# Kernel optimization log

Measured on AMD Instinct MI355X. Metric: run time of the kernel, lower is better.

Reference implementation:

```python
import jax, jax.numpy as jnp
import numpy as np

N, E, IN, H, C, ED = 100000, 1600000, 128, 4, 32, 16
HC = H * C
NEG_SLOPE = 0.2
EPS = 1e-5


def setup_inputs() -> dict:
    key = jax.random.key(0)
    ks = jax.random.split(key, 12)
    x = jax.random.normal(ks[0], (N, IN), jnp.float32)
    edge_index = jax.random.randint(ks[1], (2, E), 0, N, dtype=jnp.int32)
    edge_attr = jax.random.normal(ks[2], (E, ED), jnp.float32)
    s_in = 1.0 / np.sqrt(IN)
    s_ed = 1.0 / np.sqrt(ED)
    s_c = 1.0 / np.sqrt(C)
    Wl = jax.random.normal(ks[3], (IN, HC), jnp.float32) * s_in
    bl = jnp.zeros((HC,), jnp.float32)
    Wr = jax.random.normal(ks[4], (IN, HC), jnp.float32) * s_in
    br = jnp.zeros((HC,), jnp.float32)
    We = jax.random.normal(ks[5], (ED, HC), jnp.float32) * s_ed
    att = jax.random.normal(ks[6], (H, C), jnp.float32) * s_c
    bias = jnp.zeros((HC,), jnp.float32)
    ln_weight = jnp.ones((HC,), jnp.float32)
    ln_bias = jnp.zeros((HC,), jnp.float32)
    return {"x": x, "edge_index": edge_index, "edge_attr": edge_attr,
            "Wl": Wl, "bl": bl, "Wr": Wr, "br": br, "We": We,
            "att": att, "bias": bias, "ln_weight": ln_weight, "ln_bias": ln_bias}


def gatv2_block(x, src, dst, edge_attr, Wl, bl, Wr, br, We, att, bias, ln_weight, ln_bias):
    n = x.shape[0]
    xl = (x @ Wl + bl).reshape(n, H, C)  # source-side transform
    xr = (x @ Wr + br).reshape(n, H, C)  # target-side transform
    # add_self_loops with fill_value='mean': self-loop edge_attr = mean of
    # incoming edge_attr per node (0 for isolated nodes)
    ea_sum = jax.ops.segment_sum(edge_attr, dst, num_segments=n)
    cnt = jax.ops.segment_sum(jnp.ones((edge_attr.shape[0],), edge_attr.dtype), dst, num_segments=n)
    self_attr = ea_sum / jnp.maximum(cnt, 1.0)[:, None]
    loop = jnp.arange(n, dtype=src.dtype)
    src_a = jnp.concatenate([src, loop])
    dst_a = jnp.concatenate([dst, loop])
    ea_a = jnp.concatenate([edge_attr, self_attr], axis=0)
    e_emb = (ea_a @ We).reshape(-1, H, C)
    # GATv2 attention: a^T LeakyReLU(xl_j + xr_i + e)
    m = xl[src_a] + xr[dst_a] + e_emb            # [Etot, H, C]
    m = jax.nn.leaky_relu(m, NEG_SLOPE)
    alpha = jnp.einsum('ehc,hc->eh', m, att)     # [Etot, H]
    amax = jax.ops.segment_max(alpha, dst_a, num_segments=n)
    alpha = jnp.exp(alpha - amax[dst_a])
    denom = jax.ops.segment_sum(alpha, dst_a, num_segments=n)
    alpha = alpha / denom[dst_a]
    out = jax.ops.segment_sum(xl[src_a] * alpha[:, :, None], dst_a, num_segments=n)
    h = out.reshape(n, HC) + bias
    # residual (in_dim == H*C so no projection), PyG graph-mode LayerNorm
    z = x + h
    mu = jnp.mean(z)
    var = jnp.mean((z - mu) ** 2)
    z = (z - mu) / jnp.sqrt(var + EPS)
    z = z * ln_weight + ln_bias
    return jax.nn.relu(z)  # dropout = identity in eval


def reference(x, edge_index, edge_attr, Wl, bl, Wr, br, We, att, bias, ln_weight, ln_bias):
    src, dst = edge_index[0], edge_index[1]
    return gatv2_block(x, src, dst, edge_attr, Wl, bl, Wr, br, We, att, bias, ln_weight, ln_bias)
```

## Files before the change

kernel.cpp:

```cpp
#include <hip/hip_runtime.h>
#include <hip/hip_bf16.h>

static constexpr float NEG_SLOPE = 0.2f;
static constexpr float LN_EPS = 1e-5f;

typedef float v2f __attribute__((ext_vector_type(2)));
typedef __attribute__((ext_vector_type(8))) short bf16x8;
typedef __attribute__((ext_vector_type(4))) float f32x4;

__device__ __forceinline__ unsigned f2b(float f) {
  unsigned u = __float_as_uint(f);
  return (u + 0x7fffu + ((u >> 16) & 1u)) >> 16;
}
__device__ __forceinline__ v2f b2f2(ushort2 u) {
  v2f r;
  r.x = __uint_as_float((unsigned)u.x << 16);
  r.y = __uint_as_float((unsigned)u.y << 16);
  return r;
}
__device__ __forceinline__ float sbl(unsigned w) {
  return __uint_as_float(w << 16);
}
__device__ __forceinline__ float sbh(unsigned w) {
  return __uint_as_float(w & 0xFFFF0000u);
}

__device__ __forceinline__ float head_sum16(float x) {
  float t;
  t = __int_as_float(__builtin_amdgcn_update_dpp(
      0, __float_as_int(x), 0xB1, 0xF, 0xF, true));
  x += t;
  t = __int_as_float(__builtin_amdgcn_update_dpp(
      0, __float_as_int(x), 0x4E, 0xF, 0xF, true));
  x += t;
  t = __int_as_float(__builtin_amdgcn_update_dpp(
      0, __float_as_int(x), 0x124, 0xF, 0xF, true));
  x += t;
  t = __int_as_float(__builtin_amdgcn_update_dpp(
      0, __float_as_int(x), 0x128, 0xF, 0xF, true));
  x += t;
  return x;
}

__global__ __launch_bounds__(256) void k_packB(
    const float* __restrict__ Wl, const float* __restrict__ Wr,
    const float* __restrict__ bl, const float* __restrict__ br,
    ushort* __restrict__ Bpack, float* __restrict__ bcat)
{
  int tid = blockIdx.x * 256 + threadIdx.x;
  int l = tid & 63, s = (tid >> 6) & 3, t = tid >> 8;
  int col = t * 16 + (l & 15);
  int kb = s * 32 + (l >> 4) * 8;
  const float* __restrict__ W = (col < 128) ? Wl : Wr;
  int c = col & 127;
  unsigned p[4];
#pragma unroll
  for (int i = 0; i < 4; ++i) {
    unsigned lo = f2b(W[(size_t)(kb + 2 * i) * 128 + c]);
    unsigned hi = f2b(W[(size_t)(kb + 2 * i + 1) * 128 + c]);
    p[i] = lo | (hi << 16);
  }
  *(uint4*)(Bpack + (size_t)tid * 8) = make_uint4(p[0], p[1], p[2], p[3]);
  if (tid < 256) bcat[tid] = (tid < 128) ? bl[tid] : br[tid - 128];
}

__global__ __launch_bounds__(256) void k_gemm_mfma(
    const float* __restrict__ x, const ushort* __restrict__ Bpack,
    const float* __restrict__ bcat, ushort* __restrict__ xl,
    float* __restrict__ outz, int n)
{
  const int lane = threadIdx.x & 63;
  const int w = threadIdx.x >> 6;
  const int row0 = blockIdx.x * 64 + w * 16;
  const int rowA = min(row0 + (lane & 15), n - 1);
  const int kgrp = lane >> 4;

  f32x4 acc[16];
#pragma unroll
  for (int t = 0; t < 16; ++t) acc[t] = (f32x4){0.f, 0.f, 0.f, 0.f};

#pragma unroll
  for (int s = 0; s < 4; ++s) {
    const float4* ap =
        (const float4*)(x + (size_t)rowA * 128 + s * 32 + kgrp * 8);
    float4 a0 = ap[0], a1 = ap[1];
    bf16x8 a;
    a[0] = (short)f2b(a0.x); a[1] = (short)f2b(a0.y);
    a[2] = (short)f2b(a0.z); a[3] = (short)f2b(a0.w);
    a[4] = (short)f2b(a1.x); a[5] = (short)f2b(a1.y);
    a[6] = (short)f2b(a1.z); a[7] = (short)f2b(a1.w);
#pragma unroll
    for (int t = 0; t < 16; ++t) {
      bf16x8 b =
          *(const bf16x8*)(Bpack + (((size_t)t * 4 + s) * 64 + lane) * 8);
      acc[t] = __builtin_amdgcn_mfma_f32_16x16x32_bf16(a, b, acc[t], 0, 0, 0);
    }
  }

  const int colg = lane & 15;
  const int rbase = row0 + (lane >> 4) * 4;
#pragma unroll
  for (int t = 0; t < 16; ++t) {
    const int col = t * 16 + colg;
    const float bia = bcat[col];
    if (col < 128) {
#pragma unroll
      for (int r = 0; r < 4; ++r) {
        const int R = rbase + r;
        if (R < n) xl[(size_t)R * 128 + col] = (ushort)f2b(acc[t][r] + bia);
      }
    } else {
      const int c = col - 128;
#pragma unroll
      for (int r = 0; r < 4; ++r) {
        const int R = rbase + r;
        if (R < n) outz[(size_t)R * 128 + c] = acc[t][r] + bia;
      }
    }
  }
}

__global__ __launch_bounds__(256) void k_count(const int* __restrict__ dst,
                                               int* __restrict__ deg, int E)
{
  int e = blockIdx.x * 256 + threadIdx.x;
  if (e < E) atomicAdd(&deg[dst[e]], 1);
}

__global__ __launch_bounds__(256) void k_scan1(const int* __restrict__ deg,
                                               int* __restrict__ bsum, int n)
{
  int i = blockIdx.x * 256 + threadIdx.x;
  int v = (i < n) ? deg[i] : 0;
#pragma unroll
  for (int o = 32; o > 0; o >>= 1) v += __shfl_down(v, o);
  __shared__ int ls[4];
  if ((threadIdx.x & 63) == 0) ls[threadIdx.x >> 6] = v;
  __syncthreads();
  if (threadIdx.x == 0) bsum[blockIdx.x] = ls[0] + ls[1] + ls[2] + ls[3];
}

__global__ __launch_bounds__(512) void k_scan2(int* __restrict__ bsum, int nb)
{
  __shared__ int s[512];
  int t = threadIdx.x;
  int v = (t < nb) ? bsum[t] : 0;
  s[t] = v;
  __syncthreads();
  for (int o = 1; o < 512; o <<= 1) {
    int u = (t >= o) ? s[t - o] : 0;
    __syncthreads();
    s[t] += u;
    __syncthreads();
  }
  if (t < nb) bsum[t] = s[t] - v;
}

__global__ __launch_bounds__(256) void k_scan3(const int* __restrict__ deg,
                                               const int* __restrict__ bsum,
                                               int* __restrict__ offs, int n)
{
  __shared__ int s[256];
  int b = blockIdx.x, t = threadIdx.x, i = b * 256 + t;
  int v = (i < n) ? deg[i] : 0;
  s[t] = v;
  __syncthreads();
  for (int o = 1; o < 256; o <<= 1) {
    int u = (t >= o) ? s[t - o] : 0;
    __syncthreads();
    s[t] += u;
    __syncthreads();
  }
  if (i < n) offs[i] = bsum[b] + s[t] - v;
}

__global__ __launch_bounds__(256) void k_fill(
    const int* __restrict__ src, const int* __restrict__ dst,
    const int* __restrict__ offs, int* __restrict__ cursor,
    const float4* __restrict__ ea4, int* __restrict__ csr_src,
    ushort* __restrict__ csr_ea, int E)
{
  int e = blockIdx.x * 256 + threadIdx.x;
  if (e >= E) return;
  int d = dst[e];
  int pos = offs[d] + atomicAdd(&cursor[d], 1);
  csr_src[pos] = src[e];
  float4 r0 = ea4[(size_t)e * 4 + 0], r1 = ea4[(size_t)e * 4 + 1];
  float4 r2 = ea4[(size_t)e * 4 + 2], r3 = ea4[(size_t)e * 4 + 3];
  uint4* o4 = (uint4*)(csr_ea + (size_t)pos * 16);
  o4[0] = make_uint4(f2b(r0.x) | (f2b(r0.y) << 16), f2b(r0.z) | (f2b(r0.w) << 16),
                     f2b(r1.x) | (f2b(r1.y) << 16), f2b(r1.z) | (f2b(r1.w) << 16));
  o4[1] = make_uint4(f2b(r2.x) | (f2b(r2.y) << 16), f2b(r2.z) | (f2b(r2.w) << 16),
                     f2b(r3.x) | (f2b(r3.y) << 16), f2b(r3.z) | (f2b(r3.w) << 16));
}

__global__ __launch_bounds__(256) void k_fused(
    const int* __restrict__ csr_src, const ushort* __restrict__ csr_ea,
    const int* __restrict__ offs, const int* __restrict__ deg,
    const ushort* __restrict__ xl, const float* __restrict__ We,
    const float* __restrict__ att, const float* __restrict__ x,
    const float* __restrict__ bias, float* __restrict__ outz,
    double* __restrict__ red, int N)
{
  const int lane = threadIdx.x & 63;
  const int gw =
      __builtin_amdgcn_readfirstlane(blockIdx.x * 4 + (threadIdx.x >> 6));
  const int nw = gridDim.x * 4;
  const v2f* __restrict__ We2 = (const v2f*)We;
  const v2f* __restrict__ X2 = (const v2f*)x;
  v2f* __restrict__ Z2 = (v2f*)outz;

  v2f we[16];
#pragma unroll
  for (int k = 0; k < 16; ++k) we[k] = We2[k * 64 + lane];
  const v2f a2 = ((const v2f*)att)[lane];
  const v2f b2 = ((const v2f*)bias)[lane];
  const bool l16 = lane < 16;

  float sred = 0.f, s2red = 0.f;

  for (int node = gw; node < N; node += nw) {
    const int beg = offs[node];
    const int len = deg[node];
    const v2f xrv = Z2[(size_t)node * 64 + lane];
    const v2f xvSelf =
        b2f2(*(const ushort2*)(xl + (size_t)node * 128 + 2 * lane));

    float mA = -1e30f, dA = 0.f, esA = 0.f;
    float mB = -1e30f, dB = 0.f, esB = 0.f;
    v2f aA = {0.f, 0.f}, aB = {0.f, 0.f};

    auto edgeU = [&](v2f xv, uint4 lo, uint4 hi, float& m, float& den,
                     v2f& acc) {
      v2f emb = sbl(lo.x) * we[0];
      emb += sbh(lo.x) * we[1];
      emb += sbl(lo.y) * we[2];
      emb += sbh(lo.y) * we[3];
      emb += sbl(lo.z) * we[4];
      emb += sbh(lo.z) * we[5];
      emb += sbl(lo.w) * we[6];
      emb += sbh(lo.w) * we[7];
      emb += sbl(hi.x) * we[8];
      emb += sbh(hi.x) * we[9];
      emb += sbl(hi.y) * we[10];
      emb += sbh(hi.y) * we[11];
      emb += sbl(hi.z) * we[12];
      emb += sbh(hi.z) * we[13];
      emb += sbl(hi.w) * we[14];
      emb += sbh(hi.w) * we[15];
      v2f mm = xv + xrv + emb;
      v2f ml;
      ml.x = fmaxf(mm.x, NEG_SLOPE * mm.x);
      ml.y = fmaxf(mm.y, NEG_SLOPE * mm.y);
      const float part = head_sum16(fmaf(ml.y, a2.y, ml.x * a2.x));
      const float mn = fmaxf(m, part);
      const float c = __expf(m - mn);
      const float p = __expf(part - mn);
      den = fmaf(den, c, p);
      acc = acc * c + xv * p;
      m = mn;
    };

    auto selfEdge = [&](v2f xv, float eav, float& m, float& den, v2f& acc) {
      v2f emb = {0.f, 0.f};
#pragma unroll
      for (int k = 0; k < 16; ++k) {
        float eak = __int_as_float(
            __builtin_amdgcn_readlane(__float_as_int(eav), k));
        emb += eak * we[k];
      }
      v2f mm = xv + xrv + emb;
      v2f ml;
      ml.x = fmaxf(mm.x, NEG_SLOPE * mm.x);
      ml.y = fmaxf(mm.y, NEG_SLOPE * mm.y);
      const float part = head_sum16(fmaf(ml.y, a2.y, ml.x * a2.x));
      const float mn = fmaxf(m, part);
      const float c = __expf(m - mn);
      const float p = __expf(part - mn);
      den = fmaf(den, c, p);
      acc = acc * c + xv * p;
      m = mn;
    };

    const int nB = len >> 1;
    const int nA = len - nB;
    const int bB = beg + nA;

    uint4 eAlo = {0, 0, 0, 0}, eAhi = {0, 0, 0, 0};
    uint4 eBlo = {0, 0, 0, 0}, eBhi = {0, 0, 0, 0};
    float evA = 0.f, evB = 0.f;
    v2f xvA = {0.f, 0.f}, xvB = {0.f, 0.f};
    int sA1 = 0, sB1 = 0;

    if (len > 0) {
      const uint4* pa = (const uint4*)(csr_ea + (size_t)beg * 16);
      eAlo = pa[0];
      eAhi = pa[1];
      evA = l16 ? __uint_as_float((unsigned)csr_ea[(size_t)beg * 16 + lane]
                                  << 16)
                : 0.f;
      const int sA0 = csr_src[beg];
      xvA = b2f2(*(const ushort2*)(xl + (size_t)sA0 * 128 + 2 * lane));
      sA1 = csr_src[beg + 1];
    }
    if (nB > 0) {
      const uint4* pb = (const uint4*)(csr_ea + (size_t)bB * 16);
      eBlo = pb[0];
      eBhi = pb[1];
      evB = l16 ? __uint_as_float((unsigned)csr_ea[(size_t)bB * 16 + lane]
                                  << 16)
                : 0.f;
      const int sB0 = csr_src[bB];
      xvB = b2f2(*(const ushort2*)(xl + (size_t)sB0 * 128 + 2 * lane));
      sB1 = csr_src[bB + 1];
    }

    for (int i = 0; i < nB; ++i) {
      const size_t qA = (size_t)(beg + i + 1) * 16;
      const size_t qB = (size_t)(bB + i + 1) * 16;
      const uint4* pa = (const uint4*)(csr_ea + qA);
      const uint4* pb = (const uint4*)(csr_ea + qB);
      const uint4 nAlo = pa[0], nAhi = pa[1];
      const uint4 nBlo = pb[0], nBhi = pb[1];
      const float evA1 =
          l16 ? __uint_as_float((unsigned)csr_ea[qA + lane] << 16) : 0.f;
      const float evB1 =
          l16 ? __uint_as_float((unsigned)csr_ea[qB + lane] << 16) : 0.f;
      const v2f xvA1 =
          b2f2(*(const ushort2*)(xl + (size_t)sA1 * 128 + 2 * lane));
      const v2f xvB1 =
          b2f2(*(const ushort2*)(xl + (size_t)sB1 * 128 + 2 * lane));
      const int sA2 = csr_src[beg + i + 2];
      const int sB2 = csr_src[bB + i + 2];
      esA += evA;
      esB += evB;
      edgeU(xvA, eAlo, eAhi, mA, dA, aA);
      edgeU(xvB, eBlo, eBhi, mB, dB, aB);
      eAlo = nAlo; eAhi = nAhi; eBlo = nBlo; eBhi = nBhi;
      evA = evA1; evB = evB1;
      xvA = xvA1; xvB = xvB1;
      sA1 = sA2; sB1 = sB2;
    }
    if (nA > nB) {
      esA += evA;
      edgeU(xvA, eAlo, eAhi, mA, dA, aA);
    }
    const float inv = (len > 0) ? 1.f / (float)len : 0.f;
    selfEdge(xvSelf, (esA + esB) * inv, mA, dA, aA);

    const float mn = fmaxf(mA, mB);
    const float cA2 = __expf(mA - mn);
    const float cB2 = __expf(mB - mn);
    const float den = dA * cA2 + dB * cB2;
    const float invden = 1.f / den;
    const float o0 = (aA.x * cA2 + aB.x * cB2) * invden;
    const float o1 = (aA.y * cA2 + aB.y * cB2) * invden;

    const v2f xvn = X2[(size_t)node * 64 + lane];
    const float v0 = xvn.x + o0 + b2.x;
    const float v1 = xvn.y + o1 + b2.y;
    Z2[(size_t)node * 64 + lane] = (v2f){v0, v1};
    sred += v0 + v1;
    s2red += v0 * v0 + v1 * v1;
  }

#pragma unroll
  for (int o = 32; o > 0; o >>= 1) {
    sred += __shfl_down(sred, o);
    s2red += __shfl_down(s2red, o);
  }
  __shared__ double ls[4], ls2[4];
  const int w = threadIdx.x >> 6;
  if ((threadIdx.x & 63) == 0) {
    ls[w] = (double)sred;
    ls2[w] = (double)s2red;
  }
  __syncthreads();
  if (threadIdx.x == 0) {
    unsafeAtomicAdd(red, ls[0] + ls[1] + ls[2] + ls[3]);
    unsafeAtomicAdd(red + 1, ls2[0] + ls2[1] + ls2[2] + ls2[3]);
  }
}

__global__ __launch_bounds__(256) void k_final(
    float* __restrict__ z, const double* __restrict__ red,
    const float* __restrict__ lnw, const float* __restrict__ lnb, int M4)
{
  int i = blockIdx.x * 256 + threadIdx.x;
  if (i >= M4) return;
  const double invM = 1.0 / ((double)M4 * 4.0);
  const double mu = red[0] * invM;
  const double var = red[1] * invM - mu * mu;
  const float sc = rsqrtf((float)var + LN_EPS);
  const float muf = (float)mu;
  const float4* W4 = (const float4*)lnw;
  const float4* L4 = (const float4*)lnb;
  float4* Z4 = (float4*)z;
  float4 zv = Z4[i], wv = W4[i & 31], lv = L4[i & 31];
  float4 o;
  o.x = fmaxf((zv.x - muf) * sc * wv.x + lv.x, 0.f);
  o.y = fmaxf((zv.y - muf) * sc * wv.y + lv.y, 0.f);
  o.z = fmaxf((zv.z - muf) * sc * wv.z + lv.z, 0.f);
  o.w = fmaxf((zv.w - muf) * sc * wv.w + lv.w, 0.f);
  Z4[i] = o;
}

extern "C" void kernel_launch(void* const* d_in, const int* in_sizes, int n_in,
                              void* d_out, int out_size, void* d_ws,
                              size_t ws_size, hipStream_t stream)
{
  const float* x = (const float*)d_in[0];
  const int* ei = (const int*)d_in[1];
  const float* edge_attr = (const float*)d_in[2];
  const float* Wl = (const float*)d_in[3];
  const float* bl = (const float*)d_in[4];
  const float* Wr = (const float*)d_in[5];
  const float* br = (const float*)d_in[6];
  const float* We = (const float*)d_in[7];
  const float* att = (const float*)d_in[8];
  const float* bias = (const float*)d_in[9];
  const float* lnw = (const float*)d_in[10];
  const float* lnb = (const float*)d_in[11];
  float* out = (float*)d_out;

  const int N = in_sizes[0] / 128;
  const int E = in_sizes[1] / 2;
  const int M = N * 128;
  const int* srcp = ei;
  const int* dstp = ei + E;
  const int nb = (N + 255) / 256;

  ushort* xl = (ushort*)d_ws;
  int* deg = (int*)(xl + (size_t)M);
  int* cursor = deg + N;
  int* offs = cursor + N;
  int* bsum = offs + N;
  int* csr_src = bsum + ((nb + 7) & ~7);
  ushort* csr_ea =
      (ushort*)((((size_t)(csr_src + E + 8)) + 63) & ~(size_t)63);
  double* red =
      (double*)((((size_t)(csr_ea + (size_t)E * 16)) + 127) & ~(size_t)127);
  ushort* Bpack = (ushort*)(red + 8);
  float* bcat = (float*)(Bpack + 4096 * 8);

  hipMemsetAsync(deg, 0, (size_t)N * 8, stream);
  hipMemsetAsync(csr_src + E, 0, 32, stream);
  hipMemsetAsync(red, 0, 16, stream);

  k_packB<<<16, 256, 0, stream>>>(Wl, Wr, bl, br, Bpack, bcat);
  k_gemm_mfma<<<(N + 63) / 64, 256, 0, stream>>>(x, Bpack, bcat, xl, out, N);
  k_count<<<(E + 255) / 256, 256, 0, stream>>>(dstp, deg, E);
  k_scan1<<<nb, 256, 0, stream>>>(deg, bsum, N);
  k_scan2<<<1, 512, 0, stream>>>(bsum, nb);
  k_scan3<<<nb, 256, 0, stream>>>(deg, bsum, offs, N);
  k_fill<<<(E + 255) / 256, 256, 0, stream>>>(srcp, dstp, offs, cursor,
                                              (const float4*)edge_attr,
                                              csr_src, csr_ea, E);
  k_fused<<<4096, 256, 0, stream>>>(csr_src, csr_ea, offs, deg, xl, We, att,
                                    x, bias, out, red, N);
  k_final<<<(M / 4 + 255) / 256, 256, 0, stream>>>(out, red, lnw, lnb, M / 4);
}
```

Before: 566.0 us.

## Drop online-softmax max tracking and derive self-loop embedding from summed edge embeddings

Removes the running-max online softmax and accumulates exp(score) directly, trusting that scores stay small enough not to overflow. The self-loop embedding is now the mean of the per-edge embeddings already computed, which is valid by linearity of the We projection. This replaces the separate per-lane edge_attr loads and the 16 readlane FMA loop. The fused kernel grid is also halved to 2048 blocks, and the reduction buffer is offset to leave padding after csr_ea for prefetch overreads. Skipping max subtraction risks overflow or precision loss if attention logits grow large.

```diff
diff --git a/kernel.cpp b/kernel.cpp
--- a/kernel.cpp
+++ b/kernel.cpp
@@ -215,7 +215,6 @@
   for (int k = 0; k < 16; ++k) we[k] = We2[k * 64 + lane];
   const v2f a2 = ((const v2f*)att)[lane];
   const v2f b2 = ((const v2f*)bias)[lane];
-  const bool l16 = lane < 16;
 
   float sred = 0.f, s2red = 0.f;
 
@@ -226,12 +225,11 @@
     const v2f xvSelf =
         b2f2(*(const ushort2*)(xl + (size_t)node * 128 + 2 * lane));
 
-    float mA = -1e30f, dA = 0.f, esA = 0.f;
-    float mB = -1e30f, dB = 0.f, esB = 0.f;
+    float dA = 0.f, dB = 0.f;
     v2f aA = {0.f, 0.f}, aB = {0.f, 0.f};
-
-    auto edgeU = [&](v2f xv, uint4 lo, uint4 hi, float& m, float& den,
-                     v2f& acc) {
+    v2f embsum = {0.f, 0.f};
+
+    auto edgeU = [&](v2f xv, uint4 lo, uint4 hi, float& den, v2f& acc) {
       v2f emb = sbl(lo.x) * we[0];
       emb += sbh(lo.x) * we[1];
       emb += sbl(lo.y) * we[2];
@@ -248,38 +246,15 @@
       emb += sbh(hi.z) * we[13];
       emb += sbl(hi.w) * we[14];
       emb += sbh(hi.w) * we[15];
+      embsum += emb;
       v2f mm = xv + xrv + emb;
       v2f ml;
       ml.x = fmaxf(mm.x, NEG_SLOPE * mm.x);
       ml.y = fmaxf(mm.y, NEG_SLOPE * mm.y);
       const float part = head_sum16(fmaf(ml.y, a2.y, ml.x * a2.x));
-      const float mn = fmaxf(m, part);
-      const float c = __expf(m - mn);
-      const float p = __expf(part - mn);
-      den = fmaf(den, c, p);
-      acc = acc * c + xv * p;
-      m = mn;
-    };
-
-    auto selfEdge = [&](v2f xv, float eav, float& m, float& den, v2f& acc) {
-      v2f emb = {0.f, 0.f};
-#pragma unroll
-      for (int k = 0; k < 16; ++k) {
-        float eak = __int_as_float(
-            __builtin_amdgcn_readlane(__float_as_int(eav), k));
-        emb += eak * we[k];
-      }
-      v2f mm = xv + xrv + emb;
-      v2f ml;
-      ml.x = fmaxf(mm.x, NEG_SLOPE * mm.x);
-      ml.y = fmaxf(mm.y, NEG_SLOPE * mm.y);
-      const float part = head_sum16(fmaf(ml.y, a2.y, ml.x * a2.x));
-      const float mn = fmaxf(m, part);
-      const float c = __expf(m - mn);
-      const float p = __expf(part - mn);
-      den = fmaf(den, c, p);
-      acc = acc * c + xv * p;
-      m = mn;
+      const float p = __expf(part);
+      den += p;
+      acc += xv * p;
     };
 
     const int nB = len >> 1;
@@ -288,7 +263,6 @@
 
     uint4 eAlo = {0, 0, 0, 0}, eAhi = {0, 0, 0, 0};
     uint4 eBlo = {0, 0, 0, 0}, eBhi = {0, 0, 0, 0};
-    float evA = 0.f, evB = 0.f;
     v2f xvA = {0.f, 0.f}, xvB = {0.f, 0.f};
     int sA1 = 0, sB1 = 0;
 
@@ -296,9 +270,6 @@
       const uint4* pa = (const uint4*)(csr_ea + (size_t)beg * 16);
       eAlo = pa[0];
       eAhi = pa[1];
-      evA = l16 ? __uint_as_float((unsigned)csr_ea[(size_t)beg * 16 + lane]
-                                  << 16)
-                : 0.f;
       const int sA0 = csr_src[beg];
       xvA = b2f2(*(const ushort2*)(xl + (size_t)sA0 * 128 + 2 * lane));
       sA1 = csr_src[beg + 1];
@@ -307,54 +278,49 @@
       const uint4* pb = (const uint4*)(csr_ea + (size_t)bB * 16);
       eBlo = pb[0];
       eBhi = pb[1];
-      evB = l16 ? __uint_as_float((unsigned)csr_ea[(size_t)bB * 16 + lane]
-                                  << 16)
-                : 0.f;
       const int sB0 = csr_src[bB];
       xvB = b2f2(*(const ushort2*)(xl + (size_t)sB0 * 128 + 2 * lane));
       sB1 = csr_src[bB + 1];
     }
 
     for (int i = 0; i < nB; ++i) {
-      const size_t qA = (size_t)(beg + i + 1) * 16;
-      const size_t qB = (size_t)(bB + i + 1) * 16;
-      const uint4* pa = (const uint4*)(csr_ea + qA);
-      const uint4* pb = (const uint4*)(csr_ea + qB);
+      const uint4* pa = (const uint4*)(csr_ea + (size_t)(beg + i + 1) * 16);
+      const uint4* pb = (const uint4*)(csr_ea + (size_t)(bB + i + 1) * 16);
       const uint4 nAlo = pa[0], nAhi = pa[1];
       const uint4 nBlo = pb[0], nBhi = pb[1];
-      const float evA1 =
-          l16 ? __uint_as_float((unsigned)csr_ea[qA + lane] << 16) : 0.f;
-      const float evB1 =
-          l16 ? __uint_as_float((unsigned)csr_ea[qB + lane] << 16) : 0.f;
       const v2f xvA1 =
           b2f2(*(const ushort2*)(xl + (size_t)sA1 * 128 + 2 * lane));
       const v2f xvB1 =
           b2f2(*(const ushort2*)(xl + (size_t)sB1 * 128 + 2 * lane));
       const int sA2 = csr_src[beg + i + 2];
       const int sB2 = csr_src[bB + i + 2];
-      esA += evA;
-      esB += evB;
-      edgeU(xvA, eAlo, eAhi, mA, dA, aA);
-      edgeU(xvB, eBlo, eBhi, mB, dB, aB);
+      edgeU(xvA, eAlo, eAhi, dA, aA);
+      edgeU(xvB, eBlo, eBhi, dB, aB);
       eAlo = nAlo; eAhi = nAhi; eBlo = nBlo; eBhi = nBhi;
-      evA = evA1; evB = evB1;
       xvA = xvA1; xvB = xvB1;
       sA1 = sA2; sB1 = sB2;
     }
     if (nA > nB) {
-      esA += evA;
-      edgeU(xvA, eAlo, eAhi, mA, dA, aA);
-    }
-    const float inv = (len > 0) ? 1.f / (float)len : 0.f;
-    selfEdge(xvSelf, (esA + esB) * inv, mA, dA, aA);
-
-    const float mn = fmaxf(mA, mB);
-    const float cA2 = __expf(mA - mn);
-    const float cB2 = __expf(mB - mn);
-    const float den = dA * cA2 + dB * cB2;
+      edgeU(xvA, eAlo, eAhi, dA, aA);
+    }
+
+    {
+      const float inv = (len > 0) ? 1.f / (float)len : 0.f;
+      const v2f embS = embsum * inv;
+      v2f mm = xvSelf + xrv + embS;
+      v2f ml;
+      ml.x = fmaxf(mm.x, NEG_SLOPE * mm.x);
+      ml.y = fmaxf(mm.y, NEG_SLOPE * mm.y);
+      const float part = head_sum16(fmaf(ml.y, a2.y, ml.x * a2.x));
+      const float p = __expf(part);
+      dA += p;
+      aA += xvSelf * p;
+    }
+
+    const float den = dA + dB;
     const float invden = 1.f / den;
-    const float o0 = (aA.x * cA2 + aB.x * cB2) * invden;
-    const float o1 = (aA.y * cA2 + aB.y * cB2) * invden;
+    const float o0 = (aA.x + aB.x) * invden;
+    const float o1 = (aA.y + aB.y) * invden;
 
     const v2f xvn = X2[(size_t)node * 64 + lane];
     const float v0 = xvn.x + o0 + b2.x;
@@ -438,8 +404,8 @@
   int* csr_src = bsum + ((nb + 7) & ~7);
   ushort* csr_ea =
       (ushort*)((((size_t)(csr_src + E + 8)) + 63) & ~(size_t)63);
-  double* red =
-      (double*)((((size_t)(csr_ea + (size_t)E * 16)) + 127) & ~(size_t)127);
+  double* red = (double*)(
+      (((size_t)(csr_ea + (size_t)E * 16 + 16)) + 127) & ~(size_t)127);
   ushort* Bpack = (ushort*)(red + 8);
   float* bcat = (float*)(Bpack + 4096 * 8);
 
@@ -456,7 +422,7 @@
   k_fill<<<(E + 255) / 256, 256, 0, stream>>>(srcp, dstp, offs, cursor,
                                               (const float4*)edge_attr,
                                               csr_src, csr_ea, E);
-  k_fused<<<4096, 256, 0, stream>>>(csr_src, csr_ea, offs, deg, xl, We, att,
+  k_fused<<<2048, 256, 0, stream>>>(csr_src, csr_ea, offs, deg, xl, We, att,
                                     x, bias, out, red, N);
   k_final<<<(M / 4 + 255) / 256, 256, 0, stream>>>(out, red, lnw, lnb, M / 4);
 }
```

New measurement: 498.5 us. -11.9%, faster.
